# Kernel optimization log

Measured on AMD Instinct MI355X. Metric: run time of the kernel, lower is better.

## Reference

```python
import jax, jax.numpy as jnp
import numpy as np

THRESH = 0.5

def setup_inputs() -> dict:
    key = jax.random.key(0)
    mask = jax.random.uniform(key, (128, 1, 512, 512), dtype=jnp.float32)
    return {"mask": mask}

def _minmax_plus1(hit, full):
    # hit: [N, L] bool. Returns (min_idx, max_idx+1); (0, full) if no hit in row.
    any_hit = jnp.any(hit, axis=1)
    lo = jnp.argmax(hit, axis=1).astype(jnp.int32)
    hi = (hit.shape[1] - jnp.argmax(hit[:, ::-1], axis=1)).astype(jnp.int32)  # last hit + 1
    lo = jnp.where(any_hit, lo, jnp.int32(0))
    hi = jnp.where(any_hit, hi, jnp.int32(full))
    return lo, hi

def reference(mask):
    # mask: [N, 1, H, W] -> bbox [N, 4] = (y_min, x_min, y_max, x_max)
    m = jnp.squeeze(mask, axis=1)            # [N, H, W]
    N, H, W = m.shape
    wmat = jnp.max(m, axis=1) >= THRESH      # [N, W] column hits
    hmat = jnp.max(m, axis=2) >= THRESH      # [N, H] row hits
    xmin, xmax = _minmax_plus1(wmat, W)
    ymin, ymax = _minmax_plus1(hmat, H)
    return jnp.stack((ymin, xmin, ymax, xmax), axis=-1)  # [N, 4] int32
```

## Files before the change

kernel.cpp:

```cpp
#include <hip/hip_runtime.h>
#include <climits>


#define THRESH 0.5f

static constexpr int N = 128;
static constexpr int H = 512;
static constexpr int W = 512;
static constexpr int G = 32;
static constexpr int ROWS = H / G;
static constexpr int BLK = 256;
static constexpr int W4 = W / 4;
static constexpr int ITER = ROWS * W4 / BLK;

typedef float f32x4 __attribute__((ext_vector_type(4)));

__global__ __launch_bounds__(BLK)
void bbox_partial(const float* __restrict__ mask, int* __restrict__ partials) {
    const int n = blockIdx.x;
    const int g = blockIdx.y;
    const f32x4* base =
        (const f32x4*)(mask + (size_t)n * H * W + (size_t)g * ROWS * W);

    const int c  = threadIdx.x & (W4 - 1);
    const int rb = threadIdx.x >> 7;

    f32x4 v[ITER];
    #pragma unroll
    for (int k = 0; k < ITER; ++k)
        v[k] = __builtin_nontemporal_load(&base[threadIdx.x + k * BLK]);

    int ymin = INT_MAX, ymax = -1;
    float m0 = 0.f, m1 = 0.f, m2 = 0.f, m3 = 0.f;

    #pragma unroll
    for (int k = 0; k < ITER; ++k) {
        float mx = fmaxf(fmaxf(v[k].x, v[k].y), fmaxf(v[k].z, v[k].w));
        int r = 2 * k + rb;
        if (mx >= THRESH) { ymin = min(ymin, r); ymax = max(ymax, r); }
        m0 = fmaxf(m0, v[k].x); m1 = fmaxf(m1, v[k].y);
        m2 = fmaxf(m2, v[k].z); m3 = fmaxf(m3, v[k].w);
    }

    if (ymax >= 0) { ymin += g * ROWS; ymax += g * ROWS; }

    const int w = c << 2;
    int xmin = INT_MAX, xmax = -1;
    if (m0 >= THRESH) { xmin = w;                xmax = w;                }
    if (m1 >= THRESH) { xmin = min(xmin, w + 1); xmax = max(xmax, w + 1); }
    if (m2 >= THRESH) { xmin = min(xmin, w + 2); xmax = max(xmax, w + 2); }
    if (m3 >= THRESH) { xmin = min(xmin, w + 3); xmax = max(xmax, w + 3); }

    #pragma unroll
    for (int off = 32; off > 0; off >>= 1) {
        ymin = min(ymin, __shfl_down(ymin, off, 64));
        ymax = max(ymax, __shfl_down(ymax, off, 64));
        xmin = min(xmin, __shfl_down(xmin, off, 64));
        xmax = max(xmax, __shfl_down(xmax, off, 64));
    }

    __shared__ int s[BLK / 64][4];
    const int wave = threadIdx.x >> 6;
    const int lane = threadIdx.x & 63;
    if (lane == 0) {
        s[wave][0] = ymin; s[wave][1] = ymax; s[wave][2] = xmin; s[wave][3] = xmax;
    }
    __syncthreads();
    if (threadIdx.x == 0) {
        int a = s[0][0], b = s[0][1], cc = s[0][2], d = s[0][3];
        #pragma unroll
        for (int wv = 1; wv < BLK / 64; ++wv) {
            a  = min(a,  s[wv][0]); b = max(b, s[wv][1]);
            cc = min(cc, s[wv][2]); d = max(d, s[wv][3]);
        }
        ((int4*)partials)[n * G + g] = make_int4(a, b, cc, d);
    }
}

__global__ __launch_bounds__(128)
void bbox_final(const int* __restrict__ partials, int* __restrict__ out) {
    const int n = threadIdx.x;
    if (n >= N) return;
    int ymin = INT_MAX, ymax = -1, xmin = INT_MAX, xmax = -1;
    const int4* p = (const int4*)partials + n * G;
    #pragma unroll
    for (int g = 0; g < G; ++g) {
        int4 q = p[g];
        ymin = min(ymin, q.x); ymax = max(ymax, q.y);
        xmin = min(xmin, q.z); xmax = max(xmax, q.w);
    }
    int4 r;
    if (ymax < 0) r = make_int4(0, 0, H, W);
    else          r = make_int4(ymin, xmin, ymax + 1, xmax + 1);
    ((int4*)out)[n] = r;
}

extern "C" void kernel_launch(void* const* d_in, const int* in_sizes, int n_in,
                              void* d_out, int out_size, void* d_ws, size_t ws_size,
                              hipStream_t stream) {
    const float* mask = (const float*)d_in[0];
    int* partials = (int*)d_ws;
    int* out = (int*)d_out;

    dim3 grid(N, G);
    bbox_partial<<<grid, BLK, 0, stream>>>(mask, partials);
    bbox_final<<<1, 128, 0, stream>>>(partials, out);
}
```

Measured before the change: 176.4 us.

## Fuse final bbox reduction into partial kernel via atomics and last-block detection

Replaces the separate final reduction kernel with per-sample atomicMax accumulation of encoded min/max values and an atomic counter, so the last arriving block for each sample writes the result. The intent is to remove the second kernel launch and the partials round-trip. In exchange it adds a memset launch for workspace initialization, along with atomics whose ordering relies on a compiler barrier rather than an explicit memory fence.

```diff
diff --git a/kernel.cpp b/kernel.cpp
--- a/kernel.cpp
+++ b/kernel.cpp
@@ -16,7 +16,8 @@
 typedef float f32x4 __attribute__((ext_vector_type(4)));
 
 __global__ __launch_bounds__(BLK)
-void bbox_partial(const float* __restrict__ mask, int* __restrict__ partials) {
+void bbox_fused(const float* __restrict__ mask, int* __restrict__ enc,
+                int* __restrict__ cnt, int* __restrict__ out) {
     const int n = blockIdx.x;
     const int g = blockIdx.y;
     const f32x4* base =
@@ -66,6 +67,7 @@
         s[wave][0] = ymin; s[wave][1] = ymax; s[wave][2] = xmin; s[wave][3] = xmax;
     }
     __syncthreads();
+
     if (threadIdx.x == 0) {
         int a = s[0][0], b = s[0][1], cc = s[0][2], d = s[0][3];
         #pragma unroll
@@ -73,36 +75,44 @@
             a  = min(a,  s[wv][0]); b = max(b, s[wv][1]);
             cc = min(cc, s[wv][2]); d = max(d, s[wv][3]);
         }
-        ((int4*)partials)[n * G + g] = make_int4(a, b, cc, d);
+        const bool hit = (b >= 0);
+        const int va = hit ? (H - 1) - a  : -1;
+        const int vb = hit ? b            : -1;
+        const int vc = hit ? (W - 1) - cc : -1;
+        const int vd = hit ? d            : -1;
+
+        int* e = enc + (n << 2);
+        int d0 = atomicMax(&e[0], va);
+        int d1 = atomicMax(&e[1], vb);
+        int d2 = atomicMax(&e[2], vc);
+        int d3 = atomicMax(&e[3], vd);
+        int dep = d0 ^ d1 ^ d2 ^ d3;
+        asm volatile("" : "+v"(dep) :: "memory");
+
+        int old = atomicAdd(&cnt[n], 1);
+        if (old == G - 2) {
+            int e0 = atomicMax(&e[0], INT_MIN);
+            int e1 = atomicMax(&e[1], INT_MIN);
+            int e2 = atomicMax(&e[2], INT_MIN);
+            int e3 = atomicMax(&e[3], INT_MIN);
+            int4 r;
+            if (e1 < 0) r = make_int4(0, 0, H, W);
+            else        r = make_int4((H - 1) - e0, (W - 1) - e2, e1 + 1, e3 + 1);
+            ((int4*)out)[n] = r;
+        }
     }
-}
-
-__global__ __launch_bounds__(128)
-void bbox_final(const int* __restrict__ partials, int* __restrict__ out) {
-    const int n = threadIdx.x;
-    if (n >= N) return;
-    int ymin = INT_MAX, ymax = -1, xmin = INT_MAX, xmax = -1;
-    const int4* p = (const int4*)partials + n * G;
-    #pragma unroll
-    for (int g = 0; g < G; ++g) {
-        int4 q = p[g];
-        ymin = min(ymin, q.x); ymax = max(ymax, q.y);
-        xmin = min(xmin, q.z); xmax = max(xmax, q.w);
-    }
-    int4 r;
-    if (ymax < 0) r = make_int4(0, 0, H, W);
-    else          r = make_int4(ymin, xmin, ymax + 1, xmax + 1);
-    ((int4*)out)[n] = r;
 }
 
 extern "C" void kernel_launch(void* const* d_in, const int* in_sizes, int n_in,
                               void* d_out, int out_size, void* d_ws, size_t ws_size,
                               hipStream_t stream) {
     const float* mask = (const float*)d_in[0];
-    int* partials = (int*)d_ws;
+    int* enc = (int*)d_ws;
+    int* cnt = enc + N * 4;
     int* out = (int*)d_out;
 
+    hipMemsetAsync(d_ws, 0xFF, (size_t)(N * 5) * sizeof(int), stream);
+
     dim3 grid(N, G);
-    bbox_partial<<<grid, BLK, 0, stream>>>(mask, partials);
-    bbox_final<<<1, 128, 0, stream>>>(partials, out);
+    bbox_fused<<<grid, BLK, 0, stream>>>(mask, enc, cnt, out);
 }
```

Measured after the change: 181.6 us. 1.03x slower.
